# Optimization experiments

Hardware: AMD Instinct MI355X
Metric: run time of the kernel (lower is better)

Reference implementation:

```python
import jax, jax.numpy as jnp
import numpy as np

H = 2048          # hidden_size
I = 8192          # intermediate_size (shared expert)
E = 32            # num_experts
K = 4             # num_experts_per_tok
M = 1408          # moe_intermediate_size
B, S = 2, 1024


def setup_inputs() -> dict:
    key = jax.random.key(0)
    ks = jax.random.split(key, 7)
    scale = 0.02
    return {
        "hidden_states": jax.random.normal(ks[0], (B, S, H), dtype=jnp.float32),
        "gate_w": jax.random.normal(ks[1], (H, E), dtype=jnp.float32) * scale,
        "w1": jax.random.normal(ks[2], (E, H, M), dtype=jnp.float32) * scale,  # expert up-proj
        "w2": jax.random.normal(ks[3], (E, M, H), dtype=jnp.float32) * scale,  # expert down-proj
        "ws1": jax.random.normal(ks[4], (H, I), dtype=jnp.float32) * scale,    # shared up-proj
        "ws2": jax.random.normal(ks[5], (I, H), dtype=jnp.float32) * scale,    # shared down-proj
    }


def reference(hidden_states, gate_w, w1, w2, ws1, ws2):
    b, s, h = hidden_states.shape
    x = hidden_states.reshape(-1, h)                      # [T, H]

    # shared expert: Linear -> SiLU -> Linear
    shared = jax.nn.silu(x @ ws1) @ ws2                   # [T, H]

    # router: top-k logits, softmax over the k selected logits
    router_logits = x @ gate_w                            # [T, E]
    top_vals, top_idx = jax.lax.top_k(router_logits, K)   # [T, K]
    routing_weights = jax.nn.softmax(top_vals, axis=-1)   # [T, K]

    # combine weights: scatter top-k weights into dense [T, E]
    cw = (jax.nn.one_hot(top_idx, E, dtype=x.dtype)
          * routing_weights[..., None]).sum(axis=1)       # [T, E]

    # expert FFNs (dense over experts, weighted combine)
    a = jax.nn.silu(jnp.einsum('th,ehm->tem', x, w1))     # [T, E, M]
    expert_out = jnp.einsum('tem,emh,te->th', a, w2, cw)  # [T, H]

    output = (shared + expert_out).reshape(b, s, h)
    return output, router_logits.reshape(b, s, E)
```

## Files before the change

kernel.cpp:

```cpp
#include <hip/hip_runtime.h>

#define H_ 2048
#define E_ 32
#define KSEL 4
#define M_ 1408
#define I_ 8192
#define T_ 2048

typedef __bf16 bf16;
typedef bf16 bf16x8 __attribute__((ext_vector_type(8)));
typedef float f32x4 __attribute__((ext_vector_type(4)));
typedef unsigned short u16x8 __attribute__((ext_vector_type(8)));
typedef unsigned int u32x4 __attribute__((ext_vector_type(4)));

static __device__ __forceinline__ unsigned short bfb(float f) {
  return __builtin_bit_cast(unsigned short, (bf16)f);
}

static __device__ __forceinline__ void gload_lds16(const void* g, void* l) {
  __builtin_amdgcn_global_load_lds((const __attribute__((address_space(1))) void*)g,
                                   (__attribute__((address_space(3))) void*)l, 16, 0, 0);
}

static __device__ __forceinline__ float silu_f(float v) {
  return v / (1.f + __expf(-v));
}

static __device__ __forceinline__ void wave_argmax(float& v, int& vi) {
  #pragma unroll
  for (int off = 32; off >= 1; off >>= 1) {
    float ov = __shfl_xor(v, off);
    int   oi = __shfl_xor(vi, off);
    if (ov > v || (ov == v && oi < vi)) { v = ov; vi = oi; }
  }
}

__global__ __launch_bounds__(64) void prep_k(int* __restrict__ counts) {
  if (threadIdx.x < E_) counts[threadIdx.x] = 0;
}

__global__ __launch_bounds__(256) void cvt_k(const float* __restrict__ x, unsigned short* __restrict__ xb) {
  size_t i = ((size_t)blockIdx.x * 256 + threadIdx.x) * 8;
  float4 a = *(const float4*)(x + i);
  float4 b = *(const float4*)(x + i + 4);
  u16x8 o;
  o[0]=bfb(a.x); o[1]=bfb(a.y); o[2]=bfb(a.z); o[3]=bfb(a.w);
  o[4]=bfb(b.x); o[5]=bfb(b.y); o[6]=bfb(b.z); o[7]=bfb(b.w);
  *(u16x8*)(xb + i) = o;
}

__global__ __launch_bounds__(256) void combine_k(const float* __restrict__ sc,
                                                 const float* __restrict__ sc2,
                                                 float* __restrict__ out) {
  size_t i = ((size_t)blockIdx.x * 256 + threadIdx.x) * 4;
  int t = (int)(i >> 11);
  int h = (int)(i & 2047);
  const float* s = sc + (size_t)(t * 4) * H_ + h;
  float4 a = *(const float4*)(s);
  float4 b = *(const float4*)(s + H_);
  float4 c = *(const float4*)(s + 2 * H_);
  float4 d = *(const float4*)(s + 3 * H_);
  float4 o;
  o.x = a.x + b.x + c.x + d.x;
  o.y = a.y + b.y + c.y + d.y;
  o.z = a.z + b.z + c.z + d.z;
  o.w = a.w + b.w + c.w + d.w;
  #pragma unroll
  for (int kz = 0; kz < 4; ++kz) {
    float4 v = *(const float4*)(sc2 + (size_t)kz * T_ * H_ + i);
    o.x += v.x; o.y += v.y; o.z += v.z; o.w += v.w;
  }
  *(float4*)(out + i) = o;
}

__global__ __launch_bounds__(64) void router_k(const float* __restrict__ x, const float* __restrict__ gw,
                                               float* __restrict__ logits, int* __restrict__ counts,
                                               int* __restrict__ tlist, float* __restrict__ wlist) {
  int t = blockIdx.x;
  int l = threadIdx.x;
  int e = l & 31;
  int half = l >> 5;
  const float* xr = x + (size_t)t * H_ + half * (H_/2);
  const float* g  = gw + (size_t)(half * (H_/2)) * E_ + e;
  float a0=0.f, a1=0.f, a2=0.f, a3=0.f;
  for (int h = 0; h < H_/2; h += 4) {
    a0 = fmaf(xr[h],   g[(size_t)h*E_],     a0);
    a1 = fmaf(xr[h+1], g[(size_t)(h+1)*E_], a1);
    a2 = fmaf(xr[h+2], g[(size_t)(h+2)*E_], a2);
    a3 = fmaf(xr[h+3], g[(size_t)(h+3)*E_], a3);
  }
  float acc = (a0+a1)+(a2+a3);
  acc += __shfl_xor(acc, 32);
  if (l < E_) logits[(size_t)t*E_ + l] = acc;

  float cur = (l < E_) ? acc : -INFINITY;
  int myidx = (l < E_) ? e : 1000;
  float tv0,tv1,tv2,tv3; int ti0,ti1,ti2,ti3;
  { float v=cur; int vi=myidx; wave_argmax(v,vi); tv0=v; ti0=vi; if (myidx==vi) cur=-INFINITY; }
  { float v=cur; int vi=myidx; wave_argmax(v,vi); tv1=v; ti1=vi; if (myidx==vi) cur=-INFINITY; }
  { float v=cur; int vi=myidx; wave_argmax(v,vi); tv2=v; ti2=vi; if (myidx==vi) cur=-INFINITY; }
  { float v=cur; int vi=myidx; wave_argmax(v,vi); tv3=v; ti3=vi; }
  float w0 = 1.f;
  float w1 = __expf(tv1 - tv0);
  float w2 = __expf(tv2 - tv0);
  float w3 = __expf(tv3 - tv0);
  float inv = 1.f / (w0+w1+w2+w3);
  if (l < KSEL) {
    float myw = ((l==0)?w0:(l==1)?w1:(l==2)?w2:w3) * inv;
    int   myi = ((l==0)?ti0:(l==1)?ti1:(l==2)?ti2:ti3);
    int pos = atomicAdd(&counts[myi], 1);
    tlist[myi*T_ + pos] = (t << 2) | l;
    wlist[myi*T_ + pos] = myw;
  }
}

template<int MODE, int KDIM, int NDIM, int ASTR, int KSPLIT>
__global__ __launch_bounds__(256) void gemm_k(
    const bf16* __restrict__ A, const float* __restrict__ Bf,
    bf16* __restrict__ Cb, float* __restrict__ Cf,
    const int* __restrict__ tlist, const float* __restrict__ wlist,
    const int* __restrict__ counts)
{
  __shared__ __align__(16) char smem[12288];
  char* As = smem;
  char* Bs = smem + 8192;
  const int tid = threadIdx.x;

  int mt, nt, e = 0, kz = 0;
  int nrows = T_;
  const int* lst = nullptr;
  const float* Bp = Bf;
  if constexpr (MODE == 2 || MODE == 3) {
    constexpr int NT = NDIM / 64;
    constexpr int NWG = NT * E_ * 2;
    constexpr int CPX = NWG / 8;
    int id = blockIdx.x;
    int lg = (id & 7) * CPX + (id >> 3);
    int bit = lg & 1;
    int en  = lg >> 1;
    e  = en / NT;
    nt = en % NT;
    mt = (blockIdx.y == 0) ? bit : (2 + 2*((int)blockIdx.y - 1) + bit);
    nrows = counts[e];
    if (mt * 128 >= nrows) return;
    lst = tlist + e*T_;
    Bp = Bf + (size_t)e * ((size_t)KDIM * NDIM);
  } else {
    constexpr int NWG = 16 * (NDIM / 64);
    constexpr int CPX = NWG / 8;
    int id = blockIdx.x;
    int lg = (id & 7) * CPX + (id >> 3);
    mt = lg & 15;
    nt = lg >> 4;
    if constexpr (KSPLIT > 1) kz = blockIdx.z;
  }
  const int mrow0 = mt*128, ncol0 = nt*64;

  const bf16* abase[2];
  int aoffs[2];
  #pragma unroll
  for (int hh = 0; hh < 2; ++hh) {
    int lidx = hh*256 + tid;
    int row  = lidx >> 2;
    int slog = (lidx & 3) ^ (row & 3);
    aoffs[hh] = slog * 8;
    int ri = mrow0 + row;
    if constexpr (MODE == 2) {
      int tt = (ri < nrows) ? (lst[ri] >> 2) : 0;
      abase[hh] = A + (size_t)tt * ASTR;
    } else if constexpr (MODE == 3) {
      int ar = (ri < nrows) ? lst[ri] : 0;
      abase[hh] = A + (size_t)ar * ASTR;
    } else {
      abase[hh] = A + (size_t)ri * ASTR;
    }
  }

  const int bn = tid & 63;
  const int bq = tid >> 6;
  const float* bsrc0 = Bp + (size_t)(bq * 8) * NDIM + ncol0 + bn;
  char* const bdst = Bs + bq*1024 + bn*16;

  const int l  = tid & 63;
  const int wv = tid >> 6;
  const int wr = wv >> 1, wc = wv & 1;
  const int ss = l >> 4;

  f32x4 acc[4][2] = {};

  constexpr int ITERS = KDIM / 32 / KSPLIT;
  static_assert(ITERS % 2 == 0, "K-loop is 2-unrolled");
  const int kt0 = kz * ITERS;
  const int ktend = kt0 + ITERS;

  float vA[8], vB[8];

#define LOADB(P, KT) do {                                            \
    const float* bs_ = bsrc0 + (size_t)((KT) * 32) * NDIM;           \
    _Pragma("unroll")                                                \
    for (int j = 0; j < 8; ++j) P[j] = bs_[(size_t)j * NDIM];        \
  } while (0)

#define WRITEB(P) do {                                               \
    u32x4 w_;                                                        \
    _Pragma("unroll")                                                \
    for (int j = 0; j < 4; ++j)                                      \
      w_[j] = (unsigned)bfb(P[2*j]) | ((unsigned)bfb(P[2*j+1]) << 16); \
    *(u32x4*)(bdst) = w_;                                            \
  } while (0)

#define MFMA_PHASE() do {                                            \
    bf16x8 af[4], bfr[2];                                            \
    _Pragma("unroll")                                                \
    for (int mf = 0; mf < 4; ++mf) {                                 \
      int r = wr*64 + mf*16 + (l & 15);                              \
      af[mf] = *(const bf16x8*)(As + r*64 + ((ss ^ (r & 3)) << 4));  \
    }                                                                \
    _Pragma("unroll")                                                \
    for (int nf = 0; nf < 2; ++nf) {                                 \
      int c = wc*32 + nf*16 + (l & 15);                              \
      bfr[nf] = *(const bf16x8*)(Bs + ss*1024 + c*16);               \
    }                                                                \
    _Pragma("unroll")                                                \
    for (int mf = 0; mf < 4; ++mf)                                   \
      _Pragma("unroll")                                              \
      for (int nf = 0; nf < 2; ++nf)                                 \
        acc[mf][nf] = __builtin_amdgcn_mfma_f32_16x16x32_bf16(af[mf], bfr[nf], acc[mf][nf], 0, 0, 0); \
  } while (0)

#define ADMA(KT) do {                                                \
    _Pragma("unroll")                                                \
    for (int hh = 0; hh < 2; ++hh)                                   \
      gload_lds16(abase[hh] + (KT)*32 + aoffs[hh], As + (hh*256 + tid)*16); \
  } while (0)

  LOADB(vA, kt0);
  for (int kt = kt0; kt < ktend; kt += 2) {
    __syncthreads();
    ADMA(kt);
    WRITEB(vA);
    __syncthreads();
    LOADB(vB, kt + 1);
    MFMA_PHASE();

    __syncthreads();
    ADMA(kt + 1);
    WRITEB(vB);
    __syncthreads();
    if (kt + 2 < ktend) LOADB(vA, kt + 2);
    MFMA_PHASE();
  }

#undef LOADB
#undef WRITEB
#undef MFMA_PHASE
#undef ADMA

  #pragma unroll
  for (int mf = 0; mf < 4; ++mf) {
    #pragma unroll
    for (int j = 0; j < 4; ++j) {
      const int rloc = wr*64 + mf*16 + (l >> 4)*4 + j;
      const int grow = mrow0 + rloc;
      if constexpr (MODE == 0) {
        #pragma unroll
        for (int nf = 0; nf < 2; ++nf) {
          int col = ncol0 + wc*32 + nf*16 + (l & 15);
          Cb[(size_t)grow * NDIM + col] = (bf16)silu_f(acc[mf][nf][j]);
        }
      } else if constexpr (MODE == 1) {
        float* dst = Cf + (size_t)kz * T_ * H_;
        #pragma unroll
        for (int nf = 0; nf < 2; ++nf) {
          int col = ncol0 + wc*32 + nf*16 + (l & 15);
          dst[(size_t)grow * NDIM + col] = acc[mf][nf][j];
        }
      } else if constexpr (MODE == 2) {
        if (grow < nrows) {
          int entry = lst[grow];
          float wg = wlist[e*T_ + grow];
          #pragma unroll
          for (int nf = 0; nf < 2; ++nf) {
            int col = ncol0 + wc*32 + nf*16 + (l & 15);
            Cb[(size_t)entry * NDIM + col] = (bf16)(silu_f(acc[mf][nf][j]) * wg);
          }
        }
      } else {
        if (grow < nrows) {
          int entry = lst[grow];
          #pragma unroll
          for (int nf = 0; nf < 2; ++nf) {
            int col = ncol0 + wc*32 + nf*16 + (l & 15);
            Cf[(size_t)entry * H_ + col] = acc[mf][nf][j];
          }
        }
      }
    }
  }
}

extern "C" void kernel_launch(void* const* d_in, const int* in_sizes, int n_in,
                              void* d_out, int out_size, void* d_ws, size_t ws_size,
                              hipStream_t stream) {
  const float* x   = (const float*)d_in[0];
  const float* gw  = (const float*)d_in[1];
  const float* w1  = (const float*)d_in[2];
  const float* w2  = (const float*)d_in[3];
  const float* ws1 = (const float*)d_in[4];
  const float* ws2 = (const float*)d_in[5];
  float* out    = (float*)d_out;
  float* logits = out + (size_t)T_ * H_;

  char* ws = (char*)d_ws;
  const size_t off_xb   = 0;
  const size_t off_y1   = off_xb  + (size_t)T_ * H_ * 2;
  const size_t off_act  = off_y1  + (size_t)T_ * I_ * 2;
  const size_t off_cnt  = off_act + (size_t)T_ * 4 * M_ * 2;
  const size_t off_tl   = off_cnt + 256;
  const size_t off_wl   = off_tl  + (size_t)E_ * T_ * 4;
  const size_t off_sc   = off_wl  + (size_t)E_ * T_ * 4;
  const size_t off_sc2  = off_sc  + (size_t)T_ * 4 * H_ * 4;

  const bf16* xb = (const bf16*)(ws + off_xb);
  bf16* y1  = (bf16*)(ws + off_y1);
  bf16* act = (bf16*)(ws + off_act);
  int*  counts = (int*)(ws + off_cnt);
  int*  tlist  = (int*)(ws + off_tl);
  float* wlist = (float*)(ws + off_wl);
  float* scratch  = (float*)(ws + off_sc);
  float* scratch2 = (float*)(ws + off_sc2);

  prep_k<<<1, 64, 0, stream>>>(counts);
  router_k<<<T_, 64, 0, stream>>>(x, gw, logits, counts, tlist, wlist);
  cvt_k<<<2048, 256, 0, stream>>>(x, (unsigned short*)(ws + off_xb));

  gemm_k<0, 2048, 8192, 2048, 1><<<dim3(2048), 256, 0, stream>>>(
      xb, ws1, y1, nullptr, nullptr, nullptr, nullptr);
  gemm_k<1, 8192, 2048, 8192, 4><<<dim3(512, 1, 4), 256, 0, stream>>>(
      y1, ws2, nullptr, scratch2, nullptr, nullptr, nullptr);
  gemm_k<2, 2048, 1408, 2048, 1><<<dim3(22*E_*2, 8), 256, 0, stream>>>(
      xb, w1, act, nullptr, tlist, wlist, counts);
  gemm_k<3, 1408, 2048, 1408, 1><<<dim3(32*E_*2, 8), 256, 0, stream>>>(
      act, w2, nullptr, scratch, tlist, nullptr, counts);
  combine_k<<<4096, 256, 0, stream>>>(scratch, scratch2, out);
}
```

Measured before the change: 822.7 us.

## Triple-buffer A and fp32 B tiles via direct global-to-LDS DMA

Replaces the register-staged fp32 B loads and single-buffered A tiles with a three-stage ring of direct global_load_lds transfers for both A and the raw fp32 B tile. A per-iteration LDS convert step turns B into a double-buffered bf16 tile. Explicit vmcnt waits and sched barriers keep two tiles in flight ahead of the MFMA phase, aiming to hide global memory latency. LDS use grows from 12 KB to 56 KB per block, which can cut occupancy and adds an extra LDS round-trip for B.

```diff
diff --git a/kernel.cpp b/kernel.cpp
--- a/kernel.cpp
+++ b/kernel.cpp
@@ -121,9 +121,7 @@
     const int* __restrict__ tlist, const float* __restrict__ wlist,
     const int* __restrict__ counts)
 {
-  __shared__ __align__(16) char smem[12288];
-  char* As = smem;
-  char* Bs = smem + 8192;
+  __shared__ __align__(16) char smem[57344];
   const int tid = threadIdx.x;
 
   int mt, nt, e = 0, kz = 0;
@@ -159,27 +157,32 @@
   const bf16* abase[2];
   int aoffs[2];
   #pragma unroll
-  for (int hh = 0; hh < 2; ++hh) {
-    int lidx = hh*256 + tid;
+  for (int c = 0; c < 2; ++c) {
+    int lidx = c*256 + tid;
     int row  = lidx >> 2;
     int slog = (lidx & 3) ^ (row & 3);
-    aoffs[hh] = slog * 8;
+    aoffs[c] = slog * 8;
     int ri = mrow0 + row;
     if constexpr (MODE == 2) {
       int tt = (ri < nrows) ? (lst[ri] >> 2) : 0;
-      abase[hh] = A + (size_t)tt * ASTR;
+      abase[c] = A + (size_t)tt * ASTR;
     } else if constexpr (MODE == 3) {
       int ar = (ri < nrows) ? lst[ri] : 0;
-      abase[hh] = A + (size_t)ar * ASTR;
+      abase[c] = A + (size_t)ar * ASTR;
     } else {
-      abase[hh] = A + (size_t)ri * ASTR;
+      abase[c] = A + (size_t)ri * ASTR;
     }
+  }
+
+  const float* bbaseD[2];
+  #pragma unroll
+  for (int c = 0; c < 2; ++c) {
+    int lidx = c*256 + tid;
+    bbaseD[c] = Bp + (size_t)(lidx >> 4) * NDIM + ncol0 + (lidx & 15) * 4;
   }
 
   const int bn = tid & 63;
   const int bq = tid >> 6;
-  const float* bsrc0 = Bp + (size_t)(bq * 8) * NDIM + ncol0 + bn;
-  char* const bdst = Bs + bq*1024 + bn*16;
 
   const int l  = tid & 63;
   const int wv = tid >> 6;
@@ -189,72 +192,87 @@
   f32x4 acc[4][2] = {};
 
   constexpr int ITERS = KDIM / 32 / KSPLIT;
-  static_assert(ITERS % 2 == 0, "K-loop is 2-unrolled");
   const int kt0 = kz * ITERS;
   const int ktend = kt0 + ITERS;
 
-  float vA[8], vB[8];
-
-#define LOADB(P, KT) do {                                            \
-    const float* bs_ = bsrc0 + (size_t)((KT) * 32) * NDIM;           \
-    _Pragma("unroll")                                                \
-    for (int j = 0; j < 8; ++j) P[j] = bs_[(size_t)j * NDIM];        \
+#define SCHED0 __builtin_amdgcn_sched_barrier(0)
+#define BAR    __builtin_amdgcn_s_barrier()
+
+#define STAGE(KT, BUF) do {                                           \
+    _Pragma("unroll")                                                 \
+    for (int c = 0; c < 2; ++c)                                       \
+      gload_lds16(abase[c] + (KT)*32 + aoffs[c],                      \
+                  smem + (BUF)*8192 + (c*256 + tid)*16);              \
+    _Pragma("unroll")                                                 \
+    for (int c = 0; c < 2; ++c)                                       \
+      gload_lds16(bbaseD[c] + (size_t)(KT)*32*NDIM,                   \
+                  smem + 24576 + (BUF)*8192 + (c*256 + tid)*16);      \
   } while (0)
 
-#define WRITEB(P) do {                                               \
-    u32x4 w_;                                                        \
-    _Pragma("unroll")                                                \
-    for (int j = 0; j < 4; ++j)                                      \
-      w_[j] = (unsigned)bfb(P[2*j]) | ((unsigned)bfb(P[2*j+1]) << 16); \
-    *(u32x4*)(bdst) = w_;                                            \
+#define CVT(BUF, BB) do {                                             \
+    const char* b32_ = smem + 24576 + (BUF)*8192;                     \
+    float f_[8];                                                      \
+    _Pragma("unroll")                                                 \
+    for (int j = 0; j < 8; ++j)                                       \
+      f_[j] = *(const float*)(b32_ + (bq*8 + j)*256 + bn*4);          \
+    u32x4 w_;                                                         \
+    _Pragma("unroll")                                                 \
+    for (int j = 0; j < 4; ++j)                                       \
+      w_[j] = (unsigned)bfb(f_[2*j]) | ((unsigned)bfb(f_[2*j+1]) << 16); \
+    *(u32x4*)(smem + 49152 + (BB)*4096 + bq*1024 + bn*16) = w_;       \
   } while (0)
 
-#define MFMA_PHASE() do {                                            \
-    bf16x8 af[4], bfr[2];                                            \
-    _Pragma("unroll")                                                \
-    for (int mf = 0; mf < 4; ++mf) {                                 \
-      int r = wr*64 + mf*16 + (l & 15);                              \
-      af[mf] = *(const bf16x8*)(As + r*64 + ((ss ^ (r & 3)) << 4));  \
-    }                                                                \
-    _Pragma("unroll")                                                \
-    for (int nf = 0; nf < 2; ++nf) {                                 \
-      int c = wc*32 + nf*16 + (l & 15);                              \
-      bfr[nf] = *(const bf16x8*)(Bs + ss*1024 + c*16);               \
-    }                                                                \
-    _Pragma("unroll")                                                \
-    for (int mf = 0; mf < 4; ++mf)                                   \
-      _Pragma("unroll")                                              \
-      for (int nf = 0; nf < 2; ++nf)                                 \
+#define MFMA_PHASE(BUF, BB) do {                                      \
+    const char* As_  = smem + (BUF)*8192;                             \
+    const char* Bsb_ = smem + 49152 + (BB)*4096;                      \
+    bf16x8 af[4], bfr[2];                                             \
+    _Pragma("unroll")                                                 \
+    for (int mf = 0; mf < 4; ++mf) {                                  \
+      int r = wr*64 + mf*16 + (l & 15);                               \
+      af[mf] = *(const bf16x8*)(As_ + r*64 + ((ss ^ (r & 3)) << 4));  \
+    }                                                                 \
+    _Pragma("unroll")                                                 \
+    for (int nf = 0; nf < 2; ++nf) {                                  \
+      int c = wc*32 + nf*16 + (l & 15);                               \
+      bfr[nf] = *(const bf16x8*)(Bsb_ + ss*1024 + c*16);              \
+    }                                                                 \
+    _Pragma("unroll")                                                 \
+    for (int mf = 0; mf < 4; ++mf)                                    \
+      _Pragma("unroll")                                               \
+      for (int nf = 0; nf < 2; ++nf)                                  \
         acc[mf][nf] = __builtin_amdgcn_mfma_f32_16x16x32_bf16(af[mf], bfr[nf], acc[mf][nf], 0, 0, 0); \
   } while (0)
 
-#define ADMA(KT) do {                                                \
-    _Pragma("unroll")                                                \
-    for (int hh = 0; hh < 2; ++hh)                                   \
-      gload_lds16(abase[hh] + (KT)*32 + aoffs[hh], As + (hh*256 + tid)*16); \
-  } while (0)
-
-  LOADB(vA, kt0);
-  for (int kt = kt0; kt < ktend; kt += 2) {
-    __syncthreads();
-    ADMA(kt);
-    WRITEB(vA);
-    __syncthreads();
-    LOADB(vB, kt + 1);
-    MFMA_PHASE();
-
-    __syncthreads();
-    ADMA(kt + 1);
-    WRITEB(vB);
-    __syncthreads();
-    if (kt + 2 < ktend) LOADB(vA, kt + 2);
-    MFMA_PHASE();
-  }
-
-#undef LOADB
-#undef WRITEB
+  STAGE(kt0, 0);
+  STAGE(kt0 + 1, 1);
+  STAGE(kt0 + 2, 2);
+
+  int bi = 0, bb = 0;
+  for (int kt = kt0; kt < ktend; ++kt) {
+    const int rem = ktend - 1 - kt;
+    if (rem >= 2)      asm volatile("s_waitcnt vmcnt(8)" ::: "memory");
+    else if (rem == 1) asm volatile("s_waitcnt vmcnt(4)" ::: "memory");
+    else               asm volatile("s_waitcnt vmcnt(0)" ::: "memory");
+    SCHED0;
+    BAR;
+    CVT(bi, bb);
+    asm volatile("s_waitcnt lgkmcnt(0)" ::: "memory");
+    SCHED0;
+    BAR;
+    MFMA_PHASE(bi, bb);
+    SCHED0;
+    BAR;
+    SCHED0;
+    if (kt + 3 < ktend) STAGE(kt + 3, bi);
+    bi = (bi == 2) ? 0 : bi + 1;
+    bb ^= 1;
+  }
+
+#undef STAGE
+#undef CVT
 #undef MFMA_PHASE
-#undef ADMA
+#undef SCHED0
+#undef BAR
 
   #pragma unroll
   for (int mf = 0; mf < 4; ++mf) {
```

New measurement: 901.7 us. +9.6%, slower.
